# Performance work log

Measured on AMD Instinct MI355X. Metric: run time of the kernel, lower is better.

The kernel has to match this reference:

```python
import jax, jax.numpy as jnp
import numpy as np

N_HEAD = 16
SCALE = True
NEG = 10000.0


def setup_inputs() -> dict:
    key = jax.random.key(0)
    ks = jax.random.split(key, 5)
    B, S, D = 4, 1024, 1024
    x = jax.random.normal(ks[0], (B, S, D), dtype=jnp.float32)
    # GPT-2 Conv1D weights: W has shape [in, out], init ~N(0, 0.02)
    w_attn = jax.random.normal(ks[1], (D, 3 * D), dtype=jnp.float32) * 0.02
    b_attn = jnp.zeros((3 * D,), dtype=jnp.float32)
    w_proj = jax.random.normal(ks[2], (D, D), dtype=jnp.float32) * 0.02
    b_proj = jnp.zeros((D,), dtype=jnp.float32)
    return {"x": x, "w_attn": w_attn, "b_attn": b_attn,
            "w_proj": w_proj, "b_proj": b_proj}


def reference(x, w_attn, b_attn, w_proj, b_proj):
    B, S, D = x.shape
    H = N_HEAD
    hd = D // H
    # c_attn: Conv1D == x @ W + b
    qkv = jnp.einsum('bsd,de->bse', x, w_attn) + b_attn
    q, k, v = jnp.split(qkv, 3, axis=-1)
    # split heads -> [B, H, S, hd]
    q = q.reshape(B, S, H, hd).transpose(0, 2, 1, 3)
    k = k.reshape(B, S, H, hd).transpose(0, 2, 1, 3)
    v = v.reshape(B, S, H, hd).transpose(0, 2, 1, 3)
    # scores [B, H, S, S]
    w = jnp.einsum('bhqd,bhkd->bhqk', q, k)
    if SCALE:
        w = w / jnp.sqrt(jnp.float32(hd))
    # multiplicative causal mask: w*b - 10000*(1-b)
    bmask = jnp.tril(jnp.ones((S, S), dtype=w.dtype))[None, None]
    w = w * bmask - NEG * (1.0 - bmask)
    w = jax.nn.softmax(w, axis=-1)
    # attn_pdrop = 0 -> dropout is identity
    a = jnp.einsum('bhqk,bhkd->bhqd', w, v)
    # merge heads
    a = a.transpose(0, 2, 1, 3).reshape(B, S, D)
    # c_proj; resid_pdrop = 0
    out = jnp.einsum('bsd,de->bse', a, w_proj) + b_proj
    return out
```

## Files before the change

kernel.cpp:

```cpp
#include <hip/hip_runtime.h>
#include <hip/hip_bf16.h>


typedef __bf16 bf16x8 __attribute__((ext_vector_type(8)));
typedef __bf16 bf16x4 __attribute__((ext_vector_type(4)));
typedef float f32x4 __attribute__((ext_vector_type(4)));

__device__ __forceinline__ void load_lds16(const void* g, void* l) {
  __builtin_amdgcn_global_load_lds(
      (const __attribute__((address_space(1))) void*)g,
      (__attribute__((address_space(3))) void*)l, 16, 0, 0);
}

#define BAR8 asm volatile("s_barrier" ::: "memory")
#define LGKM0 asm volatile("s_waitcnt lgkmcnt(0)" ::: "memory")

__global__ __launch_bounds__(256) void prep(
    const float* __restrict__ x, const float* __restrict__ w_attn,
    const float* __restrict__ w_proj, __bf16* __restrict__ Xb,
    __bf16* __restrict__ WT_attn, __bf16* __restrict__ WT_proj) {
  __shared__ __bf16 tile[32][33];
  const int blk = blockIdx.x;
  const int tid = threadIdx.x;
  if (blk < 4096) {
    const float* W;
    __bf16* WT;
    int n0, k0, N;
    if (blk < 3072) {
      W = w_attn; WT = WT_attn; N = 3072;
      n0 = (blk % 96) * 32; k0 = (blk / 96) * 32;
    } else {
      W = w_proj; WT = WT_proj; N = 1024;
      const int t = blk - 3072;
      n0 = (t & 31) * 32; k0 = (t >> 5) * 32;
    }
    const int tx = tid & 31, ty = tid >> 5;
#pragma unroll
    for (int j = 0; j < 32; j += 8)
      tile[ty + j][tx] = (__bf16)W[(size_t)(k0 + ty + j) * N + n0 + tx];
    __syncthreads();
#pragma unroll
    for (int j = 0; j < 32; j += 8)
      WT[(size_t)(n0 + ty + j) * 1024 + k0 + tx] = tile[tx][ty + j];
  } else {
    const size_t i = (size_t)(blk - 4096) * 4096 + tid * 16;
    const float4* xp = (const float4*)(x + i);
    float4 a = xp[0], b = xp[1], c = xp[2], d = xp[3];
    bf16x8 o0, o1;
    o0[0] = (__bf16)a.x; o0[1] = (__bf16)a.y; o0[2] = (__bf16)a.z; o0[3] = (__bf16)a.w;
    o0[4] = (__bf16)b.x; o0[5] = (__bf16)b.y; o0[6] = (__bf16)b.z; o0[7] = (__bf16)b.w;
    o1[0] = (__bf16)c.x; o1[1] = (__bf16)c.y; o1[2] = (__bf16)c.z; o1[3] = (__bf16)c.w;
    o1[4] = (__bf16)d.x; o1[5] = (__bf16)d.y; o1[6] = (__bf16)d.z; o1[7] = (__bf16)d.w;
    *(bf16x8*)(Xb + i) = o0;
    *(bf16x8*)(Xb + i + 8) = o1;
  }
}


#define STG(GMAT, GROW0, K0, LOFF)                                             \
  _Pragma("unroll") for (int i_ = 0; i_ < 2; ++i_)                             \
    load_lds16((GMAT) + (size_t)((GROW0) + i_ * 64 + wave * 8 + srow) * 1024 + \
                   (K0) + schunk * 8,                                          \
               smem8 + (LOFF) + (i_ * 64 + wave * 8) * 64);

#define LDA8(BASE, MH)                                                         \
  _Pragma("unroll") for (int m_ = 0; m_ < 4; ++m_)                             \
  _Pragma("unroll") for (int kk_ = 0; kk_ < 2; ++kk_)                          \
    af[m_][kk_] = *(const bf16x8*)((BASE) + ((MH)*64 + m_ * 16 + l16) * 64 +   \
                                   (((kk_ * 4 + quad) ^ rsw) * 8));

#define LDB8(BASE, NLO)                                                        \
  _Pragma("unroll") for (int n_ = 0; n_ < 2; ++n_)                             \
  _Pragma("unroll") for (int kk_ = 0; kk_ < 2; ++kk_)                          \
    bf[(NLO) + n_][kk_] =                                                      \
        *(const bf16x8*)((BASE) + ((waveN & 1) * 64 + ((NLO) + n_) * 16 +      \
                                   l16) * 64 +                                 \
                         (((kk_ * 4 + quad) ^ rsw) * 8));

#define MFMA_HALF(MH, NLO)                                                     \
  __builtin_amdgcn_s_setprio(1);                                               \
  _Pragma("unroll") for (int m_ = 0; m_ < 4; ++m_)                             \
  _Pragma("unroll") for (int n_ = 0; n_ < 2; ++n_) {                           \
    acc[(MH)*4 + m_][(NLO) + n_] = __builtin_amdgcn_mfma_f32_16x16x32_bf16(    \
        af[m_][0], bf[(NLO) + n_][0], acc[(MH)*4 + m_][(NLO) + n_], 0, 0, 0);  \
    acc[(MH)*4 + m_][(NLO) + n_] = __builtin_amdgcn_mfma_f32_16x16x32_bf16(    \
        af[m_][1], bf[(NLO) + n_][1], acc[(MH)*4 + m_][(NLO) + n_], 0, 0, 0);  \
  }                                                                            \
  __builtin_amdgcn_s_setprio(0);

__global__ __launch_bounds__(512, 2) void gemm_qkv8(
    const __bf16* __restrict__ A, const __bf16* __restrict__ BT,
    const float* __restrict__ bias, __bf16* __restrict__ Qp,
    __bf16* __restrict__ Kp, __bf16* __restrict__ Vt) {
  __shared__ __bf16 smem8[65536];
  const int tid = threadIdx.x;
  const int lane = tid & 63;
  const int wave = tid >> 6;
  const int waveM = wave >> 2;
  const int waveN = wave & 3;
  const int l16 = lane & 15;
  const int quad = lane >> 4;
  const int rsw = l16 & 7;
  const int srow = lane >> 3;
  const int schunk = (lane & 7) ^ srow;

  const int bid = blockIdx.x;
  const int c = bid & 7, l = bid >> 3;
  const int tm = (c >> 1) * 4 + l / 6;
  const int tn = (c & 1) * 6 + l % 6;
  const int rowBase = tm * 256;
  const int colBase = tn * 256;

  const __bf16* aRd = smem8 + waveM * 8192;
  const __bf16* bRd = smem8 + 16384 + (waveN >> 1) * 8192;

  f32x4 acc[8][4] = {};
  bf16x8 af[4][2], bf[4][2];

  STG(A, rowBase, 0, 0);
  STG(A, rowBase + 128, 0, 8192);
  STG(BT, colBase, 0, 16384);
  STG(BT, colBase + 128, 0, 24576);
  STG(BT, colBase, 64, 32768 + 16384);
  STG(BT, colBase + 128, 64, 32768 + 24576);
  STG(A, rowBase, 64, 32768);
  asm volatile("s_waitcnt vmcnt(6)" ::: "memory");
  BAR8;

  for (int t = 0; t < 8; ++t) {
    const int kO = t * 128 + 64;
    const int kS2 = t * 128 + 128;
    const int kS3 = t * 128 + 192;
    const bool s2 = kS2 < 1024;
    const bool s3 = kS3 < 1024;

    LDA8(aRd, 0);
    LDB8(bRd, 0);
    STG(A, rowBase + 128, kO, 32768 + 8192);
    BAR8; LGKM0;
    MFMA_HALF(0, 0);
    BAR8;

    LDB8(bRd, 2);
    BAR8; LGKM0;
    MFMA_HALF(0, 2);
    BAR8;

    LDA8(aRd, 1);
    if (s2) { STG(BT, colBase, kS2, 16384); }
    BAR8; LGKM0;
    MFMA_HALF(1, 2);
    BAR8;

    if (s2) {
      STG(BT, colBase + 128, kS2, 24576);
      STG(A, rowBase, kS2, 0);
      asm volatile("s_waitcnt vmcnt(6)" ::: "memory");
    } else {
      asm volatile("s_waitcnt vmcnt(0)" ::: "memory");
    }
    BAR8;
    MFMA_HALF(1, 0);
    BAR8;

    LDA8(aRd + 32768, 0);
    LDB8(bRd + 32768, 0);
    if (s2) { STG(A, rowBase + 128, kS2, 8192); }
    BAR8; LGKM0;
    MFMA_HALF(0, 0);
    BAR8;

    LDB8(bRd + 32768, 2);
    BAR8; LGKM0;
    MFMA_HALF(0, 2);
    BAR8;

    LDA8(aRd + 32768, 1);
    if (s3) { STG(BT, colBase, kS3, 32768 + 16384); }
    BAR8; LGKM0;
    MFMA_HALF(1, 2);
    BAR8;

    if (s3) {
      STG(BT, colBase + 128, kS3, 32768 + 24576);
      STG(A, rowBase, kS3, 32768);
    }
    asm volatile("s_waitcnt vmcnt(6)" ::: "memory");
    BAR8;
    MFMA_HALF(1, 0);
    BAR8;
  }

  const int seg = colBase >> 10;
  if (seg == 2) {
#pragma unroll
    for (int mm = 0; mm < 8; ++mm) {
      const int r0 = waveM * 128 + mm * 16 + quad * 4;
#pragma unroll
      for (int n = 0; n < 4; ++n) {
        const int cR = waveN * 64 + n * 16 + l16;
        const float bv = bias[colBase + cR];
        bf16x4 pk;
#pragma unroll
        for (int r = 0; r < 4; ++r) pk[r] = (__bf16)(acc[mm][n][r] + bv);
        *(bf16x4*)(&smem8[cR * 256 + (r0 ^ (l16 << 4))]) = pk;
      }
    }
    __syncthreads();
    const int b_ = rowBase >> 10;
    const int s0 = rowBase & 1023;
    const int hBase = (colBase & 1023) >> 6;
    const int ch = lane & 31;
#pragma unroll
    for (int p = 0; p < 16; ++p) {
      const int c2 = p * 16 + wave * 2 + (lane >> 5);
      bf16x8 v =
          *(const bf16x8*)(&smem8[c2 * 256 + ((ch * 8) ^ ((c2 & 15) << 4))]);
      const int bhd = (b_ * 16 + hBase + (c2 >> 6)) * 64 + (c2 & 63);
      *(bf16x8*)(&Vt[(size_t)bhd * 1024 + s0 + ch * 8]) = v;
    }
  } else {
#pragma unroll
    for (int mm = 0; mm < 8; ++mm) {
      const int row0 = rowBase + waveM * 128 + mm * 16 + quad * 4;
#pragma unroll
      for (int n = 0; n < 4; ++n) {
        const int col = colBase + waveN * 64 + n * 16 + l16;
        const float bv = bias[col];
        const int cc = col & 1023;
        __bf16* dst = (seg == 0) ? Qp : Kp;
#pragma unroll
        for (int r = 0; r < 4; ++r) {
          const int row = row0 + r;
          const float v = acc[mm][n][r] + bv;
          const int bh = ((row >> 10) << 4) + (cc >> 6);
          dst[((size_t)bh << 16) + (size_t)(row & 1023) * 64 + (cc & 63)] =
              (__bf16)v;
        }
      }
    }
  }
}

__global__ __launch_bounds__(256) void gemm_out(
    const __bf16* __restrict__ A, const __bf16* __restrict__ BT,
    const float* __restrict__ bias, float* __restrict__ C) {
  __shared__ __bf16 sA[3][128 * 32];
  __shared__ __bf16 sB[3][128 * 32];
  const int tid = threadIdx.x;
  const int lane = tid & 63;
  const int wave = tid >> 6;
  const int waveM = wave >> 1, waveN = wave & 1;
  const int quad = lane >> 4;
  const int l16 = lane & 15;
  const int rowBase = blockIdx.x * 128;
  const int colBase = blockIdx.y * 128;
  const int rIn = lane >> 2;
  const int sIn = lane & 3;
  const int gc = sIn ^ (rIn & 3) ^ ((rIn >> 2) & 3);
  const int readSlot = quad ^ (l16 & 3) ^ ((l16 >> 2) & 3);
  f32x4 acc[4][4] = {};

#define GO_STAGE(bi, k0_)                                                      \
  _Pragma("unroll") for (int j_ = 0; j_ < 2; ++j_) {                           \
    const int rb = wave * 32 + j_ * 16;                                        \
    load_lds16(&A[(size_t)(rowBase + rb + rIn) * 1024 + (k0_) + gc * 8],       \
               &sA[bi][rb * 32]);                                              \
    load_lds16(&BT[(size_t)(colBase + rb + rIn) * 1024 + (k0_) + gc * 8],      \
               &sB[bi][rb * 32]);                                              \
  }

  GO_STAGE(0, 0);
  GO_STAGE(1, 32);
  asm volatile("s_waitcnt vmcnt(4)" ::: "memory");
  BAR8;

#pragma unroll
  for (int i = 0; i < 32; ++i) {
    if (i + 2 < 32) { GO_STAGE((i + 2) % 3, (i + 2) * 32); }
    const __bf16* sAc = sA[i % 3];
    const __bf16* sBc = sB[i % 3];
    bf16x8 af[4], bfr[4];
#pragma unroll
    for (int mt = 0; mt < 4; ++mt)
      af[mt] = *(const bf16x8*)(&sAc[(waveM * 64 + mt * 16 + l16) * 32 +
                                     readSlot * 8]);
#pragma unroll
    for (int nt = 0; nt < 4; ++nt)
      bfr[nt] = *(const bf16x8*)(&sBc[(waveN * 64 + nt * 16 + l16) * 32 +
                                      readSlot * 8]);
    __builtin_amdgcn_s_setprio(1);
#pragma unroll
    for (int mt = 0; mt < 4; ++mt)
#pragma unroll
      for (int nt = 0; nt < 4; ++nt)
        acc[mt][nt] = __builtin_amdgcn_mfma_f32_16x16x32_bf16(
            af[mt], bfr[nt], acc[mt][nt], 0, 0, 0);
    __builtin_amdgcn_s_setprio(0);
    if (i + 1 < 32) {
      if (i + 2 < 32) {
        asm volatile("s_waitcnt vmcnt(4)" ::: "memory");
      } else {
        asm volatile("s_waitcnt vmcnt(0)" ::: "memory");
      }
      BAR8;
    }
  }

#pragma unroll
  for (int mt = 0; mt < 4; ++mt) {
    const int row = rowBase + waveM * 64 + mt * 16 + quad * 4;
#pragma unroll
    for (int nt = 0; nt < 4; ++nt) {
      const int col = colBase + waveN * 64 + nt * 16 + l16;
      const float bv = bias[col];
#pragma unroll
      for (int r = 0; r < 4; ++r)
        C[(size_t)(row + r) * 1024 + col] = acc[mt][nt][r] + bv;
    }
  }
}

__global__ __launch_bounds__(256) void attn_mfma(
    const __bf16* __restrict__ Qp, const __bf16* __restrict__ Kp,
    const __bf16* __restrict__ VT, __bf16* __restrict__ Aout) {
  __shared__ __bf16 sK[2][128 * 64];
  __shared__ __bf16 sV[2][64 * 128];
  __shared__ __bf16 sP[4 * 16 * 128];

  const int tid = threadIdx.x;
  const int lane = tid & 63;
  const int wave = tid >> 6;
  const int quad = lane >> 4;
  const int l16 = lane & 15;
  const int swq = l16 & 7;

  const int bh = blockIdx.x & 63;
  const int pr = blockIdx.x >> 6;
  const int b = bh >> 4, h = bh & 15;
  const int qbA = pr * 64, qbB = (15 - pr) * 64;
  const int ktA_max = pr >> 1, ktB_max = (15 - pr) >> 1;

  const __bf16* Qb = Qp + ((size_t)bh << 16);
  const __bf16* Kb = Kp + ((size_t)bh << 16);
  const __bf16* VTb = VT + (size_t)bh * 64 * 1024;

  bf16x8 qA0A, qA1A, qA0B, qA1B;
  {
    const __bf16* qr = Qb + (size_t)(qbA + wave * 16 + l16) * 64 + quad * 8;
    qA0A = *(const bf16x8*)qr;
    qA1A = *(const bf16x8*)(qr + 32);
    qr = Qb + (size_t)(qbB + wave * 16 + l16) * 64 + quad * 8;
    qA0B = *(const bf16x8*)qr;
    qA1B = *(const bf16x8*)(qr + 32);
  }

  f32x4 OA[4] = {}, OB[4] = {};
  float psA[4] = {0.f, 0.f, 0.f, 0.f}, psB[4] = {0.f, 0.f, 0.f, 0.f};
  __bf16* pw = sP + wave * 2048;

#define ATTN_STAGE(bi, kbase)                                                  \
  _Pragma("unroll") for (int i_ = 0; i_ < 4; ++i_) {                           \
    const int rb = wave * 32 + i_ * 8;                                         \
    load_lds16(Kb + (size_t)((kbase) + rb + (lane >> 3)) * 64 +                \
                   (((lane & 7) ^ ((lane >> 3) & 7)) << 3),                    \
               &sK[bi][rb * 64]);                                              \
  }                                                                            \
  _Pragma("unroll") for (int i_ = 0; i_ < 4; ++i_) {                           \
    const int db = wave * 16 + i_ * 4;                                         \
    const int d = db + (lane >> 4);                                            \
    load_lds16(VTb + (size_t)d * 1024 + (kbase) +                              \
                   (((lane & 15) ^ (d & 7)) << 3),                             \
               &sV[bi][db * 128]);                                             \
  }

  ATTN_STAGE(0, 0);
  asm volatile("s_waitcnt vmcnt(0)" ::: "memory");
  BAR8;

  for (int kt = 0; kt <= ktB_max; ++kt) {
    const int kb = kt * 128;
    const int cur = kt & 1;
    if (kt < ktB_max) { ATTN_STAGE(cur ^ 1, kb + 128); }
    const __bf16* skc = sK[cur];
    const __bf16* svc = sV[cur];

    {
      float sc[8][4];
      __builtin_amdgcn_s_setprio(1);
#pragma unroll
      for (int n = 0; n < 8; ++n) {
        const int key = n * 16 + l16;
        bf16x8 kB0 = *(const bf16x8*)(&skc[key * 64 + ((quad ^ swq) << 3)]);
        bf16x8 kB1 = *(const bf16x8*)(&skc[key * 64 + (((quad + 4) ^ swq) << 3)]);
        f32x4 c = {};
        c = __builtin_amdgcn_mfma_f32_16x16x32_bf16(qA0B, kB0, c, 0, 0, 0);
        c = __builtin_amdgcn_mfma_f32_16x16x32_bf16(qA1B, kB1, c, 0, 0, 0);
#pragma unroll
        for (int r = 0; r < 4; ++r) sc[n][r] = c[r] * 0.125f;
      }
      __builtin_amdgcn_s_setprio(0);
      if (kt == ktB_max) {
#pragma unroll
        for (int n = 0; n < 8; ++n) {
          const int kg = kb + n * 16 + l16;
#pragma unroll
          for (int r = 0; r < 4; ++r)
            if (kg > qbB + wave * 16 + quad * 4 + r) sc[n][r] = -1.0e30f;
        }
      }
#pragma unroll
      for (int n = 0; n < 8; ++n)
#pragma unroll
        for (int r = 0; r < 4; ++r) {
          float p = __expf(fminf(sc[n][r], 60.0f));
          sc[n][r] = p;
          psB[r] += p;
        }
      {
        const int kb8 = l16 >> 3, lo = l16 & 7;
#pragma unroll
        for (int n = 0; n < 8; ++n) {
          const int chunk = n * 2 + kb8;
#pragma unroll
          for (int r = 0; r < 4; ++r) {
            const int q = quad * 4 + r;
            pw[q * 128 + ((chunk ^ (q & 7)) << 3) + lo] = (__bf16)sc[n][r];
          }
        }
      }
      __builtin_amdgcn_s_setprio(1);
#pragma unroll
      for (int cc = 0; cc < 4; ++cc) {
        bf16x8 pA = *(const bf16x8*)(&pw[l16 * 128 + (((cc * 4 + quad) ^ swq) << 3)]);
#pragma unroll
        for (int nt = 0; nt < 4; ++nt) {
          bf16x8 vB = *(const bf16x8*)(&svc[(nt * 16 + l16) * 128 +
                                            (((cc * 4 + quad) ^ swq) << 3)]);
          OB[nt] = __builtin_amdgcn_mfma_f32_16x16x32_bf16(pA, vB, OB[nt], 0, 0, 0);
        }
      }
      __builtin_amdgcn_s_setprio(0);
    }

    if (kt <= ktA_max) {
      float sc[8][4];
      __builtin_amdgcn_s_setprio(1);
#pragma unroll
      for (int n = 0; n < 8; ++n) {
        const int key = n * 16 + l16;
        bf16x8 kB0 = *(const bf16x8*)(&skc[key * 64 + ((quad ^ swq) << 3)]);
        bf16x8 kB1 = *(const bf16x8*)(&skc[key * 64 + (((quad + 4) ^ swq) << 3)]);
        f32x4 c = {};
        c = __builtin_amdgcn_mfma_f32_16x16x32_bf16(qA0A, kB0, c, 0, 0, 0);
        c = __builtin_amdgcn_mfma_f32_16x16x32_bf16(qA1A, kB1, c, 0, 0, 0);
#pragma unroll
        for (int r = 0; r < 4; ++r) sc[n][r] = c[r] * 0.125f;
      }
      __builtin_amdgcn_s_setprio(0);
      if (kt == ktA_max) {
#pragma unroll
        for (int n = 0; n < 8; ++n) {
          const int kg = kb + n * 16 + l16;
#pragma unroll
          for (int r = 0; r < 4; ++r)
            if (kg > qbA + wave * 16 + quad * 4 + r) sc[n][r] = -1.0e30f;
        }
      }
#pragma unroll
      for (int n = 0; n < 8; ++n)
#pragma unroll
        for (int r = 0; r < 4; ++r) {
          float p = __expf(fminf(sc[n][r], 60.0f));
          sc[n][r] = p;
          psA[r] += p;
        }
      {
        const int kb8 = l16 >> 3, lo = l16 & 7;
#pragma unroll
        for (int n = 0; n < 8; ++n) {
          const int chunk = n * 2 + kb8;
#pragma unroll
          for (int r = 0; r < 4; ++r) {
            const int q = quad * 4 + r;
            pw[q * 128 + ((chunk ^ (q & 7)) << 3) + lo] = (__bf16)sc[n][r];
          }
        }
      }
      __builtin_amdgcn_s_setprio(1);
#pragma unroll
      for (int cc = 0; cc < 4; ++cc) {
        bf16x8 pA = *(const bf16x8*)(&pw[l16 * 128 + (((cc * 4 + quad) ^ swq) << 3)]);
#pragma unroll
        for (int nt = 0; nt < 4; ++nt) {
          bf16x8 vB = *(const bf16x8*)(&svc[(nt * 16 + l16) * 128 +
                                            (((cc * 4 + quad) ^ swq) << 3)]);
          OA[nt] = __builtin_amdgcn_mfma_f32_16x16x32_bf16(pA, vB, OA[nt], 0, 0, 0);
        }
      }
      __builtin_amdgcn_s_setprio(0);
    }

    if (kt < ktB_max) {
      asm volatile("s_waitcnt vmcnt(0)" ::: "memory");
      BAR8;
    }
  }

  float invA[4], invB[4];
#pragma unroll
  for (int r = 0; r < 4; ++r) {
    float pa = psA[r], pb = psB[r];
    pa += __shfl_xor(pa, 1); pb += __shfl_xor(pb, 1);
    pa += __shfl_xor(pa, 2); pb += __shfl_xor(pb, 2);
    pa += __shfl_xor(pa, 4); pb += __shfl_xor(pb, 4);
    pa += __shfl_xor(pa, 8); pb += __shfl_xor(pb, 8);
    invA[r] = 1.0f / pa;
    invB[r] = 1.0f / pb;
  }
#pragma unroll
  for (int nt = 0; nt < 4; ++nt) {
#pragma unroll
    for (int r = 0; r < 4; ++r) {
      const int qA = qbA + wave * 16 + quad * 4 + r;
      const int qB = qbB + wave * 16 + quad * 4 + r;
      Aout[((size_t)b * 1024 + qA) * 1024 + h * 64 + nt * 16 + l16] =
          (__bf16)(OA[nt][r] * invA[r]);
      Aout[((size_t)b * 1024 + qB) * 1024 + h * 64 + nt * 16 + l16] =
          (__bf16)(OB[nt][r] * invB[r]);
    }
  }
}

extern "C" void kernel_launch(void* const* d_in, const int* in_sizes, int n_in,
                              void* d_out, int out_size, void* d_ws,
                              size_t ws_size, hipStream_t stream) {
  const float* x      = (const float*)d_in[0];
  const float* w_attn = (const float*)d_in[1];
  const float* b_attn = (const float*)d_in[2];
  const float* w_proj = (const float*)d_in[3];
  const float* b_proj = (const float*)d_in[4];
  float* out = (float*)d_out;

  char* ws = (char*)d_ws;
  __bf16* WT_attn = (__bf16*)(ws);
  __bf16* WT_proj = (__bf16*)(ws + 6291456);
  __bf16* Xb      = (__bf16*)(ws + 8388608);
  __bf16* Qp      = (__bf16*)(ws + 16777216);
  __bf16* Kp      = (__bf16*)(ws + 25165824);
  __bf16* VT      = (__bf16*)(ws + 33554432);
  __bf16* Aattn   = (__bf16*)(ws + 41943040);

  prep<<<5120, 256, 0, stream>>>(x, w_attn, w_proj, Xb, WT_attn, WT_proj);
  gemm_qkv8<<<192, 512, 0, stream>>>(Xb, WT_attn, b_attn, Qp, Kp, VT);
  attn_mfma<<<512, 256, 0, stream>>>(Qp, Kp, VT, Aattn);
  gemm_out<<<dim3(32, 8), 256, 0, stream>>>(Aattn, WT_proj, b_proj, out);
}
```

Before: 164.9 us.

## Split paired attention blocks into single-tile blocks reading K/V directly from global

The attention kernel no longer pairs a light and a heavy query tile per block; each of 1024 blocks handles one 64-row query tile, ordered heaviest first. K and V are read straight from global memory into registers instead of being staged through double-buffered LDS, which removes the barriers and most of the LDS use so more blocks fit per CU (launch bounds raised to 4). Separately, the Q/K epilogue of the QKV GEMM now stages results through shared memory so they can be written to global as 16-byte vectors instead of scattered scalar stores. The trade-off is that K/V tiles are no longer shared through LDS across waves, so each wave reloads them from global or cache, and block imbalance now depends on the scheduler.

```diff
diff --git a/kernel.cpp b/kernel.cpp
--- a/kernel.cpp
+++ b/kernel.cpp
@@ -220,24 +220,34 @@
       *(bf16x8*)(&Vt[(size_t)bhd * 1024 + s0 + ch * 8]) = v;
     }
   } else {
+    __bf16* dst = (seg == 0) ? Qp : Kp;
 #pragma unroll
     for (int mm = 0; mm < 8; ++mm) {
-      const int row0 = rowBase + waveM * 128 + mm * 16 + quad * 4;
 #pragma unroll
       for (int n = 0; n < 4; ++n) {
-        const int col = colBase + waveN * 64 + n * 16 + l16;
-        const float bv = bias[col];
-        const int cc = col & 1023;
-        __bf16* dst = (seg == 0) ? Qp : Kp;
+        const int colL = waveN * 64 + n * 16 + l16;
+        const float bv = bias[colBase + colL];
 #pragma unroll
         for (int r = 0; r < 4; ++r) {
-          const int row = row0 + r;
-          const float v = acc[mm][n][r] + bv;
-          const int bh = ((row >> 10) << 4) + (cc >> 6);
-          dst[((size_t)bh << 16) + (size_t)(row & 1023) * 64 + (cc & 63)] =
-              (__bf16)v;
+          const int rowL = waveM * 128 + mm * 16 + quad * 4 + r;
+          smem8[rowL * 256 + (colL ^ (((rowL >> 2) & 3) << 4))] =
+              (__bf16)(acc[mm][n][r] + bv);
         }
       }
+    }
+    __syncthreads();
+#pragma unroll
+    for (int p = 0; p < 16; ++p) {
+      const int chunk = p * 512 + tid;
+      const int rowL = chunk >> 5;
+      const int colL0 = (chunk & 31) * 8;
+      bf16x8 v = *(const bf16x8*)(
+          &smem8[rowL * 256 + (colL0 ^ (((rowL >> 2) & 3) << 4))]);
+      const int row = rowBase + rowL;
+      const int cc = (colBase + colL0) & 1023;
+      const int bh = ((row >> 10) << 4) + (cc >> 6);
+      *(bf16x8*)(&dst[((size_t)bh << 16) + (size_t)(row & 1023) * 64 +
+                      (cc & 63)]) = v;
     }
   }
 }
@@ -321,11 +331,9 @@
   }
 }
 
-__global__ __launch_bounds__(256) void attn_mfma(
+__global__ __launch_bounds__(256, 4) void attn_mfma(
     const __bf16* __restrict__ Qp, const __bf16* __restrict__ Kp,
     const __bf16* __restrict__ VT, __bf16* __restrict__ Aout) {
-  __shared__ __bf16 sK[2][128 * 64];
-  __shared__ __bf16 sV[2][64 * 128];
   __shared__ __bf16 sP[4 * 16 * 128];
 
   const int tid = threadIdx.x;
@@ -336,198 +344,106 @@
   const int swq = l16 & 7;
 
   const int bh = blockIdx.x & 63;
-  const int pr = blockIdx.x >> 6;
+  const int qt = 15 - (blockIdx.x >> 6);
   const int b = bh >> 4, h = bh & 15;
-  const int qbA = pr * 64, qbB = (15 - pr) * 64;
-  const int ktA_max = pr >> 1, ktB_max = (15 - pr) >> 1;
+  const int qb = qt * 64;
+  const int ktmax = qt >> 1;
 
   const __bf16* Qb = Qp + ((size_t)bh << 16);
   const __bf16* Kb = Kp + ((size_t)bh << 16);
   const __bf16* VTb = VT + (size_t)bh * 64 * 1024;
 
-  bf16x8 qA0A, qA1A, qA0B, qA1B;
+  bf16x8 qA0, qA1;
   {
-    const __bf16* qr = Qb + (size_t)(qbA + wave * 16 + l16) * 64 + quad * 8;
-    qA0A = *(const bf16x8*)qr;
-    qA1A = *(const bf16x8*)(qr + 32);
-    qr = Qb + (size_t)(qbB + wave * 16 + l16) * 64 + quad * 8;
-    qA0B = *(const bf16x8*)qr;
-    qA1B = *(const bf16x8*)(qr + 32);
-  }
-
-  f32x4 OA[4] = {}, OB[4] = {};
-  float psA[4] = {0.f, 0.f, 0.f, 0.f}, psB[4] = {0.f, 0.f, 0.f, 0.f};
+    const __bf16* qr = Qb + (size_t)(qb + wave * 16 + l16) * 64 + quad * 8;
+    qA0 = *(const bf16x8*)qr;
+    qA1 = *(const bf16x8*)(qr + 32);
+  }
+
+  f32x4 O[4] = {};
+  float ps[4] = {0.f, 0.f, 0.f, 0.f};
   __bf16* pw = sP + wave * 2048;
 
-#define ATTN_STAGE(bi, kbase)                                                  \
-  _Pragma("unroll") for (int i_ = 0; i_ < 4; ++i_) {                           \
-    const int rb = wave * 32 + i_ * 8;                                         \
-    load_lds16(Kb + (size_t)((kbase) + rb + (lane >> 3)) * 64 +                \
-                   (((lane & 7) ^ ((lane >> 3) & 7)) << 3),                    \
-               &sK[bi][rb * 64]);                                              \
-  }                                                                            \
-  _Pragma("unroll") for (int i_ = 0; i_ < 4; ++i_) {                           \
-    const int db = wave * 16 + i_ * 4;                                         \
-    const int d = db + (lane >> 4);                                            \
-    load_lds16(VTb + (size_t)d * 1024 + (kbase) +                              \
-                   (((lane & 15) ^ (d & 7)) << 3),                             \
-               &sV[bi][db * 128]);                                             \
-  }
-
-  ATTN_STAGE(0, 0);
-  asm volatile("s_waitcnt vmcnt(0)" ::: "memory");
-  BAR8;
-
-  for (int kt = 0; kt <= ktB_max; ++kt) {
+  for (int kt = 0; kt <= ktmax; ++kt) {
     const int kb = kt * 128;
-    const int cur = kt & 1;
-    if (kt < ktB_max) { ATTN_STAGE(cur ^ 1, kb + 128); }
-    const __bf16* skc = sK[cur];
-    const __bf16* svc = sV[cur];
+    float sc[8][4];
+
+    __builtin_amdgcn_s_setprio(1);
+#pragma unroll
+    for (int n = 0; n < 8; ++n) {
+      const __bf16* kr = Kb + (size_t)(kb + n * 16 + l16) * 64 + quad * 8;
+      bf16x8 kB0 = *(const bf16x8*)kr;
+      bf16x8 kB1 = *(const bf16x8*)(kr + 32);
+      f32x4 cacc = {};
+      cacc = __builtin_amdgcn_mfma_f32_16x16x32_bf16(qA0, kB0, cacc, 0, 0, 0);
+      cacc = __builtin_amdgcn_mfma_f32_16x16x32_bf16(qA1, kB1, cacc, 0, 0, 0);
+#pragma unroll
+      for (int r = 0; r < 4; ++r) sc[n][r] = cacc[r] * 0.125f;
+    }
+    __builtin_amdgcn_s_setprio(0);
+
+    if (kt == ktmax) {
+#pragma unroll
+      for (int n = 0; n < 8; ++n) {
+        const int kg = kb + n * 16 + l16;
+#pragma unroll
+        for (int r = 0; r < 4; ++r)
+          if (kg > qb + wave * 16 + quad * 4 + r) sc[n][r] = -1.0e30f;
+      }
+    }
+
+#pragma unroll
+    for (int n = 0; n < 8; ++n)
+#pragma unroll
+      for (int r = 0; r < 4; ++r) {
+        float p = __expf(fminf(sc[n][r], 60.0f));
+        sc[n][r] = p;
+        ps[r] += p;
+      }
 
     {
-      float sc[8][4];
-      __builtin_amdgcn_s_setprio(1);
+      const int kb8 = l16 >> 3, lo = l16 & 7;
 #pragma unroll
       for (int n = 0; n < 8; ++n) {
-        const int key = n * 16 + l16;
-        bf16x8 kB0 = *(const bf16x8*)(&skc[key * 64 + ((quad ^ swq) << 3)]);
-        bf16x8 kB1 = *(const bf16x8*)(&skc[key * 64 + (((quad + 4) ^ swq) << 3)]);
-        f32x4 c = {};
-        c = __builtin_amdgcn_mfma_f32_16x16x32_bf16(qA0B, kB0, c, 0, 0, 0);
-        c = __builtin_amdgcn_mfma_f32_16x16x32_bf16(qA1B, kB1, c, 0, 0, 0);
-#pragma unroll
-        for (int r = 0; r < 4; ++r) sc[n][r] = c[r] * 0.125f;
-      }
-      __builtin_amdgcn_s_setprio(0);
-      if (kt == ktB_max) {
-#pragma unroll
-        for (int n = 0; n < 8; ++n) {
-          const int kg = kb + n * 16 + l16;
-#pragma unroll
-          for (int r = 0; r < 4; ++r)
-            if (kg > qbB + wave * 16 + quad * 4 + r) sc[n][r] = -1.0e30f;
+        const int chunk = n * 2 + kb8;
+#pragma unroll
+        for (int r = 0; r < 4; ++r) {
+          const int q = quad * 4 + r;
+          pw[q * 128 + ((chunk ^ (q & 7)) << 3) + lo] = (__bf16)sc[n][r];
         }
       }
-#pragma unroll
-      for (int n = 0; n < 8; ++n)
-#pragma unroll
-        for (int r = 0; r < 4; ++r) {
-          float p = __expf(fminf(sc[n][r], 60.0f));
-          sc[n][r] = p;
-          psB[r] += p;
-        }
-      {
-        const int kb8 = l16 >> 3, lo = l16 & 7;
-#pragma unroll
-        for (int n = 0; n < 8; ++n) {
-          const int chunk = n * 2 + kb8;
-#pragma unroll
-          for (int r = 0; r < 4; ++r) {
-            const int q = quad * 4 + r;
-            pw[q * 128 + ((chunk ^ (q & 7)) << 3) + lo] = (__bf16)sc[n][r];
-          }
-        }
-      }
-      __builtin_amdgcn_s_setprio(1);
-#pragma unroll
-      for (int cc = 0; cc < 4; ++cc) {
-        bf16x8 pA = *(const bf16x8*)(&pw[l16 * 128 + (((cc * 4 + quad) ^ swq) << 3)]);
-#pragma unroll
-        for (int nt = 0; nt < 4; ++nt) {
-          bf16x8 vB = *(const bf16x8*)(&svc[(nt * 16 + l16) * 128 +
-                                            (((cc * 4 + quad) ^ swq) << 3)]);
-          OB[nt] = __builtin_amdgcn_mfma_f32_16x16x32_bf16(pA, vB, OB[nt], 0, 0, 0);
-        }
-      }
-      __builtin_amdgcn_s_setprio(0);
-    }
-
-    if (kt <= ktA_max) {
-      float sc[8][4];
-      __builtin_amdgcn_s_setprio(1);
-#pragma unroll
-      for (int n = 0; n < 8; ++n) {
-        const int key = n * 16 + l16;
-        bf16x8 kB0 = *(const bf16x8*)(&skc[key * 64 + ((quad ^ swq) << 3)]);
-        bf16x8 kB1 = *(const bf16x8*)(&skc[key * 64 + (((quad + 4) ^ swq) << 3)]);
-        f32x4 c = {};
-        c = __builtin_amdgcn_mfma_f32_16x16x32_bf16(qA0A, kB0, c, 0, 0, 0);
-        c = __builtin_amdgcn_mfma_f32_16x16x32_bf16(qA1A, kB1, c, 0, 0, 0);
-#pragma unroll
-        for (int r = 0; r < 4; ++r) sc[n][r] = c[r] * 0.125f;
-      }
-      __builtin_amdgcn_s_setprio(0);
-      if (kt == ktA_max) {
-#pragma unroll
-        for (int n = 0; n < 8; ++n) {
-          const int kg = kb + n * 16 + l16;
-#pragma unroll
-          for (int r = 0; r < 4; ++r)
-            if (kg > qbA + wave * 16 + quad * 4 + r) sc[n][r] = -1.0e30f;
-        }
-      }
-#pragma unroll
-      for (int n = 0; n < 8; ++n)
-#pragma unroll
-        for (int r = 0; r < 4; ++r) {
-          float p = __expf(fminf(sc[n][r], 60.0f));
-          sc[n][r] = p;
-          psA[r] += p;
-        }
-      {
-        const int kb8 = l16 >> 3, lo = l16 & 7;
-#pragma unroll
-        for (int n = 0; n < 8; ++n) {
-          const int chunk = n * 2 + kb8;
-#pragma unroll
-          for (int r = 0; r < 4; ++r) {
-            const int q = quad * 4 + r;
-            pw[q * 128 + ((chunk ^ (q & 7)) << 3) + lo] = (__bf16)sc[n][r];
-          }
-        }
-      }
-      __builtin_amdgcn_s_setprio(1);
-#pragma unroll
-      for (int cc = 0; cc < 4; ++cc) {
-        bf16x8 pA = *(const bf16x8*)(&pw[l16 * 128 + (((cc * 4 + quad) ^ swq) << 3)]);
-#pragma unroll
-        for (int nt = 0; nt < 4; ++nt) {
-          bf16x8 vB = *(const bf16x8*)(&svc[(nt * 16 + l16) * 128 +
-                                            (((cc * 4 + quad) ^ swq) << 3)]);
-          OA[nt] = __builtin_amdgcn_mfma_f32_16x16x32_bf16(pA, vB, OA[nt], 0, 0, 0);
-        }
-      }
-      __builtin_amdgcn_s_setprio(0);
-    }
-
-    if (kt < ktB_max) {
-      asm volatile("s_waitcnt vmcnt(0)" ::: "memory");
-      BAR8;
-    }
-  }
-
-  float invA[4], invB[4];
+    }
+    __builtin_amdgcn_s_setprio(1);
+#pragma unroll
+    for (int cc = 0; cc < 4; ++cc) {
+      bf16x8 pA = *(const bf16x8*)(&pw[l16 * 128 + (((cc * 4 + quad) ^ swq) << 3)]);
+#pragma unroll
+      for (int nt = 0; nt < 4; ++nt) {
+        bf16x8 vB = *(const bf16x8*)(VTb + (size_t)(nt * 16 + l16) * 1024 +
+                                     kb + (cc * 4 + quad) * 8);
+        O[nt] = __builtin_amdgcn_mfma_f32_16x16x32_bf16(pA, vB, O[nt], 0, 0, 0);
+      }
+    }
+    __builtin_amdgcn_s_setprio(0);
+  }
+
+  float inv[4];
 #pragma unroll
   for (int r = 0; r < 4; ++r) {
-    float pa = psA[r], pb = psB[r];
-    pa += __shfl_xor(pa, 1); pb += __shfl_xor(pb, 1);
-    pa += __shfl_xor(pa, 2); pb += __shfl_xor(pb, 2);
-    pa += __shfl_xor(pa, 4); pb += __shfl_xor(pb, 4);
-    pa += __shfl_xor(pa, 8); pb += __shfl_xor(pb, 8);
-    invA[r] = 1.0f / pa;
-    invB[r] = 1.0f / pb;
+    float pa = ps[r];
+    pa += __shfl_xor(pa, 1);
+    pa += __shfl_xor(pa, 2);
+    pa += __shfl_xor(pa, 4);
+    pa += __shfl_xor(pa, 8);
+    inv[r] = 1.0f / pa;
   }
 #pragma unroll
   for (int nt = 0; nt < 4; ++nt) {
 #pragma unroll
     for (int r = 0; r < 4; ++r) {
-      const int qA = qbA + wave * 16 + quad * 4 + r;
-      const int qB = qbB + wave * 16 + quad * 4 + r;
-      Aout[((size_t)b * 1024 + qA) * 1024 + h * 64 + nt * 16 + l16] =
-          (__bf16)(OA[nt][r] * invA[r]);
-      Aout[((size_t)b * 1024 + qB) * 1024 + h * 64 + nt * 16 + l16] =
-          (__bf16)(OB[nt][r] * invB[r]);
+      const int q = qb + wave * 16 + quad * 4 + r;
+      Aout[((size_t)b * 1024 + q) * 1024 + h * 64 + nt * 16 + l16] =
+          (__bf16)(O[nt][r] * inv[r]);
     }
   }
 }
@@ -553,6 +469,6 @@
 
   prep<<<5120, 256, 0, stream>>>(x, w_attn, w_proj, Xb, WT_attn, WT_proj);
   gemm_qkv8<<<192, 512, 0, stream>>>(Xb, WT_attn, b_attn, Qp, Kp, VT);
-  attn_mfma<<<512, 256, 0, stream>>>(Qp, Kp, VT, Aattn);
+  attn_mfma<<<1024, 256, 0, stream>>>(Qp, Kp, VT, Aattn);
   gemm_out<<<dim3(32, 8), 256, 0, stream>>>(Aattn, WT_proj, b_proj, out);
 }
```

Result: slower. 221.8 us (+34.5%).
